# Kernel tuning notes

Hardware: AMD Instinct MI355X
Metric: run time of the kernel (lower is better)

The kernel has to match this reference:

```python
import jax, jax.numpy as jnp
import numpy as np

N_NODES = 50000


def _gine(x, src, dst, edge_embed, lin_w, lin_b, nn_w, nn_b):
    # PyG GINEConv (eps=0): out = nn(x + sum_{j->i} ReLU(x_j + lin(edge_attr)))
    e = edge_embed @ lin_w + lin_b              # [E, d_in]
    msg = jax.nn.relu(x[src] + e)               # gather + fuse, [E, d_in]
    agg = jax.ops.segment_sum(msg, dst, num_segments=N_NODES)  # scatter-add, [N, d_in]
    return (x + agg) @ nn_w + nn_b              # small MLP, [N, d_out]


def setup_inputs() -> dict:
    key = jax.random.key(0)
    ks = jax.random.split(key, 20)
    E = 800000
    h = 128
    sc = lambda f_in: 1.0 / np.sqrt(f_in)
    inp = {
        "x": jax.random.normal(ks[0], (N_NODES, 1), jnp.float32),
        "edge_index": jax.random.randint(ks[1], (2, E), 0, N_NODES, jnp.int64),
        "edge_attr": jax.random.normal(ks[2], (E, 1), jnp.float32),
        "em_w": jax.random.normal(ks[3], (1, h), jnp.float32) * sc(1),
        "em_b": jnp.zeros((h,), jnp.float32),
        "l1_w": jax.random.normal(ks[4], (h, 1), jnp.float32) * sc(h),
        "l1_b": jnp.zeros((1,), jnp.float32),
        "n1_w": jax.random.normal(ks[5], (1, h), jnp.float32) * sc(1),
        "n1_b": jnp.zeros((h,), jnp.float32),
        "l2_w": jax.random.normal(ks[6], (h, h), jnp.float32) * sc(h),
        "l2_b": jnp.zeros((h,), jnp.float32),
        "n2_w": jax.random.normal(ks[7], (h, h), jnp.float32) * sc(h),
        "n2_b": jnp.zeros((h,), jnp.float32),
        "l3_w": jax.random.normal(ks[8], (h, h), jnp.float32) * sc(h),
        "l3_b": jnp.zeros((h,), jnp.float32),
        "n3_w": jax.random.normal(ks[9], (h, h), jnp.float32) * sc(h),
        "n3_b": jnp.zeros((h,), jnp.float32),
        "dec_w": jax.random.normal(ks[10], (2 * h, 1), jnp.float32) * sc(2 * h),
        "dec_b": jnp.zeros((1,), jnp.float32),
    }
    return inp


def reference(x, edge_index, edge_attr, em_w, em_b, l1_w, l1_b, n1_w, n1_b,
              l2_w, l2_b, n2_w, n2_b, l3_w, l3_b, n3_w, n3_b, dec_w, dec_b):
    src, dst = edge_index[0], edge_index[1]
    edge_embed = edge_attr @ em_w + em_b                      # [E, 128]
    hdn = _gine(x,   src, dst, edge_embed, l1_w, l1_b, n1_w, n1_b)
    hdn = _gine(hdn, src, dst, edge_embed, l2_w, l2_b, n2_w, n2_b)
    hdn = _gine(hdn, src, dst, edge_embed, l3_w, l3_b, n3_w, n3_b)
    h_cat = jnp.concatenate([hdn[src], hdn[dst]], axis=-1)    # [E, 256]
    return h_cat @ dec_w + dec_b                              # [E, 1]
```

## Files before the change

kernel.cpp:

```cpp
#include <hip/hip_runtime.h>

#define H 128
#define CAPC 3072


typedef unsigned long long ull;
using bf16x8 = __attribute__((ext_vector_type(8))) short;
using f32x4  = __attribute__((ext_vector_type(4))) float;

__device__ __forceinline__ float bf2f(unsigned short v) {
  return __uint_as_float(((unsigned)v) << 16);
}
__device__ __forceinline__ unsigned short bf16r(float v) {
  unsigned u = __float_as_uint(v);
  u = (u + 0x7FFFu + ((u >> 16) & 1u)) >> 16;
  return (unsigned short)u;
}
__device__ __forceinline__ unsigned bf16pair(float a, float b) {
  return (unsigned)bf16r(a) | ((unsigned)bf16r(b) << 16);
}

__global__ __launch_bounds__(256) void init_consts(
    const float* __restrict__ em_w, const float* __restrict__ em_b,
    const float* __restrict__ l1_w, const float* __restrict__ l1_b,
    const float* __restrict__ l2_w, const float* __restrict__ l2_b,
    const float* __restrict__ n1_b,
    const float* __restrict__ l3_w, const float* __restrict__ l3_b,
    const float* __restrict__ n2w, const float* __restrict__ n3w,
    const float* __restrict__ n3b, const float* __restrict__ dec_w,
    float* __restrict__ consts, int* __restrict__ cursor,
    unsigned short* __restrict__ w2t) {
  if (blockIdx.x > 0) {
    const int i = (blockIdx.x - 1) * 256 + threadIdx.x;
    if (i < H * H) {
      const int j = i >> 7, k = i & (H - 1);
      w2t[k * H + j] = bf16r(n2w[i]);
    }
    return;
  }
  const int k = threadIdx.x;
  cursor[k] = 0;
  cursor[k + 256] = 0;
  __shared__ float sa[H], sc[H];
  if (k < H) {
    float u2 = 0.f, c2 = 0.f, u3 = 0.f, c3 = 0.f, vA = 0.f, vB = 0.f;
    for (int j = 0; j < H; ++j) {
      const float ew = em_w[j], eb = em_b[j];
      u2 = fmaf(ew, l2_w[j * H + k], u2);
      c2 = fmaf(eb, l2_w[j * H + k], c2);
      u3 = fmaf(ew, l3_w[j * H + k], u3);
      c3 = fmaf(eb, l3_w[j * H + k], c3);
      vA = fmaf(n3w[k * H + j], dec_w[j], vA);
      vB = fmaf(n3w[k * H + j], dec_w[H + j], vB);
    }
    consts[2 + k]         = u2;
    consts[2 + H + k]     = c2 + l2_b[k] + n1_b[k];
    consts[2 + 2 * H + k] = u3;
    consts[2 + 3 * H + k] = c3 + l3_b[k];
    consts[514 + k]       = vA;
    consts[642 + k]       = vB;
    sa[k] = em_w[k] * l1_w[k];
    sc[k] = em_b[k] * l1_w[k];
  }
  __syncthreads();
  for (int s = 64; s > 0; s >>= 1) {
    if (k < s) { sa[k] += sa[k + s]; sc[k] += sc[k + s]; }
    __syncthreads();
  }
  if (k == 0) { consts[0] = sa[0]; consts[1] = sc[0] + l1_b[0]; }
  __syncthreads();
  if (k < H) {
    sa[k] = n3b[k] * dec_w[k];
    sc[k] = n3b[k] * dec_w[H + k];
  }
  __syncthreads();
  for (int s = 64; s > 0; s >>= 1) {
    if (k < s) { sa[k] += sa[k + s]; sc[k] += sc[k + s]; }
    __syncthreads();
  }
  if (k == 0) { consts[770] = sa[0]; consts[771] = sc[0]; }
}

__global__ __launch_bounds__(1024) void bin_scatter(
    const int* __restrict__ src, const int* __restrict__ dst,
    const float* __restrict__ ea, int* __restrict__ cursor,
    ull* __restrict__ spc, int E, int NBUCK) {
  __shared__ int lhist[512];
  __shared__ int lbase[512];
  const int tid = threadIdx.x;
  const int base = blockIdx.x * 2048 + tid * 2;
  if (tid < 512) lhist[tid] = 0;
  __syncthreads();
  int s_[2], d_[2], b_[2], r_[2];
  float a_[2];
#pragma unroll
  for (int j = 0; j < 2; ++j) {
    const int e = base + j;
    if (e < E) {
      s_[j] = src[e]; d_[j] = dst[e]; a_[j] = ea[e];
      b_[j] = d_[j] >> 7;
      r_[j] = atomicAdd(&lhist[b_[j]], 1);
    } else {
      b_[j] = -1;
    }
  }
  __syncthreads();
  if (tid < NBUCK && lhist[tid] > 0)
    lbase[tid] = atomicAdd(&cursor[tid], lhist[tid]);
  __syncthreads();
#pragma unroll
  for (int j = 0; j < 2; ++j) {
    if (b_[j] >= 0) {
      const int pl = lbase[b_[j]] + r_[j];
      if (pl < CAPC)
        spc[(size_t)b_[j] * CAPC + pl] =
            ((ull)(unsigned)(s_[j] | ((d_[j] & 127) << 16)) << 32) |
            (ull)(unsigned)__float_as_uint(a_[j]);
    }
  }
}

__global__ __launch_bounds__(1024) void fine_scatter(
    const int* __restrict__ cursor, const ull* __restrict__ spc,
    const float* __restrict__ x, const float* __restrict__ consts,
    int2* __restrict__ spf, int* __restrict__ rowstart,
    float* __restrict__ s1, int N) {
  __shared__ int lh[128];
  __shared__ int sd[128];
  __shared__ int cur[128];
  __shared__ int2 pay[CAPC];
  const int tid = threadIdx.x;
  const int b = blockIdx.x;
  const int cnt = min(cursor[b], CAPC);
  const size_t rbase = (size_t)b * CAPC;
  if (tid < 128) lh[tid] = 0;
  __syncthreads();
  for (int i = tid; i < cnt; i += 1024)
    atomicAdd(&lh[(int)((spc[rbase + i] >> 48) & 127u)], 1);
  __syncthreads();
  if (tid < 128) sd[tid] = lh[tid];
  __syncthreads();
  for (int off = 1; off < 128; off <<= 1) {
    int t = 0;
    if (tid < 128 && tid >= off) t = sd[tid - off];
    __syncthreads();
    if (tid < 128) sd[tid] += t;
    __syncthreads();
  }
  if (tid < 128) {
    const int ex = sd[tid] - lh[tid];
    cur[tid] = ex;
    rowstart[b * 129 + tid] = (int)rbase + ex;
    if (tid == 0) rowstart[b * 129 + 128] = (int)rbase + cnt;
  }
  __syncthreads();
  for (int i = tid; i < cnt; i += 1024) {
    const ull payv = spc[rbase + i];
    const int dl = (int)((payv >> 48) & 127u);
    const int pos = atomicAdd(&cur[dl], 1);
    pay[pos] = make_int2((int)((payv >> 32) & 0xFFFFu), (int)(unsigned)payv);
  }
  __syncthreads();
  for (int i = tid; i < cnt; i += 1024) spf[rbase + i] = pay[i];
  const int lane = tid & 63, w = tid >> 6;
  const float a1 = consts[0], c1 = consts[1];
  for (int i = w; i < 128; i += 16) {
    const int n = (b << 7) + i;
    if (n >= N) break;
    const int rsl = sd[i] - lh[i], ci = lh[i];
    float part = 0.f;
    for (int j = lane; j < ci; j += 64) {
      const int2 pv = pay[rsl + j];
      part += fmaxf(x[pv.x] + fmaf(a1, __int_as_float(pv.y), c1), 0.f);
    }
#pragma unroll
    for (int o = 32; o >= 1; o >>= 1) part += __shfl_xor(part, o, 64);
    if (lane == 0) s1[n] = x[n] + part;
  }
}

__global__ __launch_bounds__(256) void layer2_wave(
    const int* __restrict__ rowstart, const int2* __restrict__ sp,
    const float* __restrict__ s1, const float* __restrict__ n1w,
    const float* __restrict__ n1b, const float* __restrict__ consts,
    const unsigned short* __restrict__ w2t, const float* __restrict__ n2b,
    unsigned short* __restrict__ h2b, int N) {
  __shared__ unsigned short t2s[4][16][136];
  const int tid = threadIdx.x, w = tid >> 6, lane = tid & 63;
  const int node0 = (blockIdx.x * 4 + w) * 16;
  {
    const float w0 = n1w[lane],            w1 = n1w[lane + 64];
    const float u0 = consts[2 + lane],     u1 = consts[2 + lane + 64];
    const float c0 = consts[2 + H + lane], c1 = consts[2 + H + lane + 64];
    const float b0 = n1b[lane],            b1 = n1b[lane + 64];
    for (int m = 0; m < 16; ++m) {
      const int n = node0 + m;
      if (n < N) {
        const int rb = (n >> 7) * 129 + (n & 127);
        const int rs = rowstart[rb], re = rowstart[rb + 1];
        float acc0 = 0.f, acc1 = 0.f;
        for (int base = rs; base < re; base += 64) {
          const int i = base + lane;
          float s1v = 0.f, eav = 0.f;
          if (i < re) {
            const int2 sv = sp[i];
            s1v = s1[sv.x];
            eav = __int_as_float(sv.y);
          }
          const int cntv = min(64, re - base);
          for (int j = 0; j < cntv; ++j) {
            const float s = __shfl(s1v, j, 64);
            const float a = __shfl(eav, j, 64);
            acc0 += fmaxf(fmaf(s, w0, fmaf(a, u0, c0)), 0.f);
            acc1 += fmaxf(fmaf(s, w1, fmaf(a, u1, c1)), 0.f);
          }
        }
        const float sn = s1[n];
        t2s[w][m][lane]      = bf16r(fmaf(sn, w0, b0) + acc0);
        t2s[w][m][lane + 64] = bf16r(fmaf(sn, w1, b1) + acc1);
      } else {
        t2s[w][m][lane] = 0;
        t2s[w][m][lane + 64] = 0;
      }
    }
  }
  __builtin_amdgcn_wave_barrier();
  const int col = lane & 15, quad = lane >> 4;
  const bf16x8 a0 = *(const bf16x8*)&t2s[w][col][quad * 8];
  const bf16x8 a1 = *(const bf16x8*)&t2s[w][col][32 + quad * 8];
  const bf16x8 a2 = *(const bf16x8*)&t2s[w][col][64 + quad * 8];
  const bf16x8 a3 = *(const bf16x8*)&t2s[w][col][96 + quad * 8];
  float hv[8][4];
#pragma unroll
  for (int t = 0; t < 8; ++t) {
    const bf16x8* bcol =
        (const bf16x8*)(w2t + (size_t)(t * 16 + col) * H + quad * 8);
    f32x4 acc = {0.f, 0.f, 0.f, 0.f};
    acc = __builtin_amdgcn_mfma_f32_16x16x32_bf16(a0, bcol[0], acc, 0, 0, 0);
    acc = __builtin_amdgcn_mfma_f32_16x16x32_bf16(a1, bcol[4], acc, 0, 0, 0);
    acc = __builtin_amdgcn_mfma_f32_16x16x32_bf16(a2, bcol[8], acc, 0, 0, 0);
    acc = __builtin_amdgcn_mfma_f32_16x16x32_bf16(a3, bcol[12], acc, 0, 0, 0);
    const float bias = n2b[t * 16 + col];
#pragma unroll
    for (int r = 0; r < 4; ++r) hv[t][r] = acc[r] + bias;
  }
  __builtin_amdgcn_wave_barrier();
#pragma unroll
  for (int t = 0; t < 8; ++t)
#pragma unroll
    for (int r = 0; r < 4; ++r)
      t2s[w][quad * 4 + r][t * 16 + col] = bf16r(hv[t][r]);
  __builtin_amdgcn_wave_barrier();
#pragma unroll
  for (int m = 0; m < 16; ++m) {
    const int n = node0 + m;
    if (n < N)
      ((unsigned*)h2b)[(size_t)n * 64 + lane] =
          *(const unsigned*)&t2s[w][m][2 * lane];
  }
}

__global__ __launch_bounds__(256) void layer3_dot(
    const int* __restrict__ rowstart, const int2* __restrict__ sp,
    const unsigned short* __restrict__ h2b, const float* __restrict__ consts,
    float* __restrict__ p, float* __restrict__ q, int N) {
  const int n = (blockIdx.x * blockDim.x + threadIdx.x) >> 6;
  const int lane = threadIdx.x & 63;
  if (n >= N) return;
  const int k0 = 2 * lane;
  const float u0 = consts[2 + 2 * H + k0], u1 = consts[2 + 2 * H + k0 + 1];
  const float c0 = consts[2 + 3 * H + k0], c1 = consts[2 + 3 * H + k0 + 1];
  const float vA0 = consts[514 + k0], vA1 = consts[514 + k0 + 1];
  const float vB0 = consts[642 + k0], vB1 = consts[642 + k0 + 1];
  const int rb = (n >> 7) * 129 + (n & 127);
  const int rs = rowstart[rb], re = rowstart[rb + 1];
  float acc0 = 0.f, acc1 = 0.f;
  for (int base = rs; base < re; base += 64) {
    const int i = base + lane;
    int esrc = 0;
    float eav = 0.f;
    if (i < re) {
      const int2 sv = sp[i];
      esrc = sv.x;
      eav = __int_as_float(sv.y);
    }
    const int cntv = min(64, re - base);
    int j = 0;
    for (; j + 4 <= cntv; j += 4) {
      const int s0 = __shfl(esrc, j, 64),     s1i = __shfl(esrc, j + 1, 64);
      const int s2 = __shfl(esrc, j + 2, 64), s3 = __shfl(esrc, j + 3, 64);
      const float a0 = __shfl(eav, j, 64),     a1 = __shfl(eav, j + 1, 64);
      const float a2 = __shfl(eav, j + 2, 64), a3 = __shfl(eav, j + 3, 64);
      const ushort2 h0 = *(const ushort2*)&h2b[(size_t)s0 * H + k0];
      const ushort2 h1 = *(const ushort2*)&h2b[(size_t)s1i * H + k0];
      const ushort2 h2v = *(const ushort2*)&h2b[(size_t)s2 * H + k0];
      const ushort2 h3 = *(const ushort2*)&h2b[(size_t)s3 * H + k0];
      acc0 += fmaxf(bf2f(h0.x) + fmaf(a0, u0, c0), 0.f);
      acc1 += fmaxf(bf2f(h0.y) + fmaf(a0, u1, c1), 0.f);
      acc0 += fmaxf(bf2f(h1.x) + fmaf(a1, u0, c0), 0.f);
      acc1 += fmaxf(bf2f(h1.y) + fmaf(a1, u1, c1), 0.f);
      acc0 += fmaxf(bf2f(h2v.x) + fmaf(a2, u0, c0), 0.f);
      acc1 += fmaxf(bf2f(h2v.y) + fmaf(a2, u1, c1), 0.f);
      acc0 += fmaxf(bf2f(h3.x) + fmaf(a3, u0, c0), 0.f);
      acc1 += fmaxf(bf2f(h3.y) + fmaf(a3, u1, c1), 0.f);
    }
    for (; j < cntv; ++j) {
      const int s0 = __shfl(esrc, j, 64);
      const float a0 = __shfl(eav, j, 64);
      const ushort2 hv = *(const ushort2*)&h2b[(size_t)s0 * H + k0];
      acc0 += fmaxf(bf2f(hv.x) + fmaf(a0, u0, c0), 0.f);
      acc1 += fmaxf(bf2f(hv.y) + fmaf(a0, u1, c1), 0.f);
    }
  }
  const ushort2 hn = *(const ushort2*)&h2b[(size_t)n * H + k0];
  const float t0 = bf2f(hn.x) + acc0;
  const float t1 = bf2f(hn.y) + acc1;
  float pd = t0 * vA0 + t1 * vA1;
  float qd = t0 * vB0 + t1 * vB1;
#pragma unroll
  for (int o = 32; o >= 1; o >>= 1) {
    pd += __shfl_xor(pd, o, 64);
    qd += __shfl_xor(qd, o, 64);
  }
  if (lane == 0) {
    p[n] = pd + consts[770];
    q[n] = qd + consts[771];
  }
}

__global__ void final_kernel(const int* __restrict__ src,
                             const int* __restrict__ dst,
                             const float* __restrict__ p,
                             const float* __restrict__ q,
                             const float* __restrict__ dec_b,
                             float* __restrict__ out, int E) {
  const int e = blockIdx.x * blockDim.x + threadIdx.x;
  if (e < E) out[e] = p[src[e]] + q[dst[e]] + dec_b[0];
}

extern "C" void kernel_launch(void* const* d_in, const int* in_sizes, int n_in,
                              void* d_out, int out_size, void* d_ws, size_t ws_size,
                              hipStream_t stream) {
  const float* x     = (const float*)d_in[0];
  const int*   ei    = (const int*)d_in[1];
  const float* ea    = (const float*)d_in[2];
  const float* em_w  = (const float*)d_in[3];
  const float* em_b  = (const float*)d_in[4];
  const float* l1_w  = (const float*)d_in[5];
  const float* l1_b  = (const float*)d_in[6];
  const float* n1_w  = (const float*)d_in[7];
  const float* n1_b  = (const float*)d_in[8];
  const float* l2_w  = (const float*)d_in[9];
  const float* l2_b  = (const float*)d_in[10];
  const float* n2_w  = (const float*)d_in[11];
  const float* n2_b  = (const float*)d_in[12];
  const float* l3_w  = (const float*)d_in[13];
  const float* l3_b  = (const float*)d_in[14];
  const float* n3_w  = (const float*)d_in[15];
  const float* n3_b  = (const float*)d_in[16];
  const float* dec_w = (const float*)d_in[17];
  const float* dec_b = (const float*)d_in[18];
  float* out = (float*)d_out;

  const int N = in_sizes[0];
  const int E = in_sizes[2];
  const int* src = ei;
  const int* dst = ei + E;

  const int NBUCK  = (N + 127) >> 7;
  const int NBATCH = (E + 2047) >> 11;
  const int NPAD   = ((N + 15) / 16) * 16;
  const int NB64   = (N + 63) / 64;

  float* ws       = (float*)d_ws;
  float* consts   = ws;
  ull*   spc      = (ull*)(ws + 1024);
  int2*  spf      = (int2*)(spc + (size_t)NBUCK * CAPC);
  unsigned short* h2b = (unsigned short*)(spf + (size_t)NBUCK * CAPC);
  unsigned short* w2t = h2b + (size_t)NPAD * H;
  float* s1       = (float*)(w2t + H * H);
  float* p        = s1 + N;
  float* q        = p + N;
  int*   cursor   = (int*)(q + N);
  int*   rowstart = cursor + 512;

  init_consts<<<65, 256, 0, stream>>>(em_w, em_b, l1_w, l1_b, l2_w, l2_b,
                                      n1_b, l3_w, l3_b, n2_w, n3_w, n3_b,
                                      dec_w, consts, cursor, w2t);
  bin_scatter<<<NBATCH, 1024, 0, stream>>>(src, dst, ea, cursor, spc, E, NBUCK);
  fine_scatter<<<NBUCK, 1024, 0, stream>>>(cursor, spc, x, consts, spf,
                                           rowstart, s1, N);
  layer2_wave<<<NB64, 256, 0, stream>>>(rowstart, spf, s1, n1_w, n1_b,
                                        consts, w2t, n2_b, h2b, N);
  layer3_dot<<<(N + 3) / 4, 256, 0, stream>>>(rowstart, spf, h2b, consts,
                                              p, q, N);
  final_kernel<<<(E + 255) / 256, 256, 0, stream>>>(src, dst, p, q, dec_b, out, E);
}
```

Measured before the change: 228.5 us.

## Stream layer-2 edges across 16 nodes per wave with next-chunk prefetch

In layer2_wave the per-node edge loop is replaced by one contiguous walk over all edges of the wave's 16 nodes. Edges are loaded 64 at a time and the next chunk is prefetched while the current one is processed. Node boundaries are tracked from a shuffled copy of the rowstart values, and each node's result is flushed to shared memory when its range ends. With about 16 edges per node, the old loop left most lanes idle on each load and serialized one dependent load round per node; the new loop fills the loads and overlaps them with compute, at the cost of a data-dependent boundary check inside the inner loop.

```diff
diff --git a/kernel.cpp b/kernel.cpp
--- a/kernel.cpp
+++ b/kernel.cpp
@@ -188,41 +188,64 @@
   __shared__ unsigned short t2s[4][16][136];
   const int tid = threadIdx.x, w = tid >> 6, lane = tid & 63;
   const int node0 = (blockIdx.x * 4 + w) * 16;
+  if (node0 >= N) return;
+  const float w0 = n1w[lane],            w1 = n1w[lane + 64];
+  const float u0 = consts[2 + lane],     u1 = consts[2 + lane + 64];
+  const float c0 = consts[2 + H + lane], c1 = consts[2 + H + lane + 64];
+  const float b0 = n1b[lane],            b1 = n1b[lane + 64];
+  const int rb0 = ((node0 >> 7) * 129) + (node0 & 127);
+  int rbv = 0;
+  if (lane <= 16) rbv = rowstart[rb0 + lane];
+  float s1v16 = 0.f;
+  if (lane < 16 && node0 + lane < N) s1v16 = s1[node0 + lane];
+  const int rs = __shfl(rbv, 0, 64);
+  const int re = __shfl(rbv, 16, 64);
+  int cur = 0;
+  int rend_cur = __shfl(rbv, 1, 64);
+  float acc0 = 0.f, acc1 = 0.f;
+  float eav = 0.f, s1e = 0.f;
   {
-    const float w0 = n1w[lane],            w1 = n1w[lane + 64];
-    const float u0 = consts[2 + lane],     u1 = consts[2 + lane + 64];
-    const float c0 = consts[2 + H + lane], c1 = consts[2 + H + lane + 64];
-    const float b0 = n1b[lane],            b1 = n1b[lane + 64];
-    for (int m = 0; m < 16; ++m) {
-      const int n = node0 + m;
-      if (n < N) {
-        const int rb = (n >> 7) * 129 + (n & 127);
-        const int rs = rowstart[rb], re = rowstart[rb + 1];
-        float acc0 = 0.f, acc1 = 0.f;
-        for (int base = rs; base < re; base += 64) {
-          const int i = base + lane;
-          float s1v = 0.f, eav = 0.f;
-          if (i < re) {
-            const int2 sv = sp[i];
-            s1v = s1[sv.x];
-            eav = __int_as_float(sv.y);
-          }
-          const int cntv = min(64, re - base);
-          for (int j = 0; j < cntv; ++j) {
-            const float s = __shfl(s1v, j, 64);
-            const float a = __shfl(eav, j, 64);
-            acc0 += fmaxf(fmaf(s, w0, fmaf(a, u0, c0)), 0.f);
-            acc1 += fmaxf(fmaf(s, w1, fmaf(a, u1, c1)), 0.f);
-          }
-        }
-        const float sn = s1[n];
-        t2s[w][m][lane]      = bf16r(fmaf(sn, w0, b0) + acc0);
-        t2s[w][m][lane + 64] = bf16r(fmaf(sn, w1, b1) + acc1);
-      } else {
-        t2s[w][m][lane] = 0;
-        t2s[w][m][lane + 64] = 0;
+    const int i0 = rs + lane;
+    if (i0 < re) {
+      const int2 sv = sp[i0];
+      eav = __int_as_float(sv.y);
+      s1e = s1[sv.x];
+    }
+  }
+  for (int base = rs; base < re; base += 64) {
+    float nav = 0.f, ns1 = 0.f;
+    {
+      const int inext = base + 64 + lane;
+      if (inext < re) {
+        const int2 sv = sp[inext];
+        nav = __int_as_float(sv.y);
+        ns1 = s1[sv.x];
       }
     }
+    const int cntv = min(64, re - base);
+    for (int j = 0; j < cntv; ++j) {
+      const int gi = base + j;
+      while (gi >= rend_cur) {
+        const float sn = __shfl(s1v16, cur, 64);
+        t2s[w][cur][lane]      = bf16r(fmaf(sn, w0, b0) + acc0);
+        t2s[w][cur][lane + 64] = bf16r(fmaf(sn, w1, b1) + acc1);
+        acc0 = 0.f; acc1 = 0.f;
+        ++cur;
+        rend_cur = __shfl(rbv, cur + 1, 64);
+      }
+      const float s = __shfl(s1e, j, 64);
+      const float a = __shfl(eav, j, 64);
+      acc0 += fmaxf(fmaf(s, w0, fmaf(a, u0, c0)), 0.f);
+      acc1 += fmaxf(fmaf(s, w1, fmaf(a, u1, c1)), 0.f);
+    }
+    eav = nav; s1e = ns1;
+  }
+  while (cur < 16) {
+    const float sn = __shfl(s1v16, cur, 64);
+    t2s[w][cur][lane]      = bf16r(fmaf(sn, w0, b0) + acc0);
+    t2s[w][cur][lane + 64] = bf16r(fmaf(sn, w1, b1) + acc1);
+    acc0 = 0.f; acc1 = 0.f;
+    ++cur;
   }
   __builtin_amdgcn_wave_barrier();
   const int col = lane & 15, quad = lane >> 4;
```

After: 248.2 us. 8.6% more time.
